# Kernel tuning notes

Measured on AMD Instinct MI355X. Metric: run time of the kernel, lower is better.

## Reference

```python
import jax, jax.numpy as jnp
import numpy as np

# Multi-scale feature pyramid (H, W) per level, standard Deformable-DETR for ~800x800 input
SHAPES = [(100, 100), (50, 50), (25, 25), (13, 13)]
D = 256      # d_model
NH = 8       # n_heads
NL = 4       # n_levels
NP = 4       # n_points
HD = D // NH # head_dim = 32
B = 2
S = sum(h * w for h, w in SHAPES)  # 13294
Lq = S  # encoder-style: one query per multi-scale token


def setup_inputs() -> dict:
    key = jax.random.key(0)
    ks = jax.random.split(key, 11)
    return {
        "query": jax.random.normal(ks[0], (B, Lq, D), jnp.float32),
        "reference_points": jax.random.uniform(ks[1], (B, Lq, NL, 2), jnp.float32),
        "value": jax.random.normal(ks[2], (B, S, D), jnp.float32),
        "W_val": jax.random.normal(ks[3], (D, D), jnp.float32) * 0.02,
        "b_val": jnp.zeros((D,), jnp.float32),
        "W_off": jax.random.normal(ks[4], (D, NH * NL * NP * 2), jnp.float32) * 0.01,
        "b_off": jax.random.normal(ks[5], (NH * NL * NP * 2,), jnp.float32) * 0.5,
        "W_attn": jax.random.normal(ks[6], (D, NH * NL * NP), jnp.float32) * 0.02,
        "b_attn": jnp.zeros((NH * NL * NP,), jnp.float32),
        "W_out": jax.random.normal(ks[7], (D, D), jnp.float32) * 0.02,
        "b_out": jnp.zeros((D,), jnp.float32),
    }


def _bilinear_sample(valf, x, y, H, W):
    """grid_sample(mode=bilinear, padding_mode=zeros, align_corners=False).
    valf: [N, H*W, C] flattened feature map; x, y: [N, P] pixel-space coords
    (already converted via x = loc_x*W - 0.5). Returns [N, P, C].
    """
    x0 = jnp.floor(x); y0 = jnp.floor(y)
    x1 = x0 + 1.0;     y1 = y0 + 1.0
    wx1 = x - x0; wx0 = 1.0 - wx1
    wy1 = y - y0; wy0 = 1.0 - wy1

    def corner(xi, yi, w):
        inb = (xi >= 0) & (xi <= W - 1) & (yi >= 0) & (yi <= H - 1)
        xi_c = jnp.clip(xi, 0, W - 1).astype(jnp.int32)
        yi_c = jnp.clip(yi, 0, H - 1).astype(jnp.int32)
        idx = yi_c * W + xi_c                                   # [N, P]
        v = jnp.take_along_axis(valf, idx[..., None], axis=1)   # [N, P, C]
        return v * (w * inb.astype(valf.dtype))[..., None]

    return (corner(x0, y0, wx0 * wy0) + corner(x1, y0, wx1 * wy0)
            + corner(x0, y1, wx0 * wy1) + corner(x1, y1, wx1 * wy1))


def reference(query, reference_points, value, W_val, b_val, W_off, b_off,
              W_attn, b_attn, W_out, b_out):
    Bq, L, _ = query.shape
    # value projection, split into heads: [B, S, NH, HD]
    val = (value @ W_val + b_val).reshape(Bq, S, NH, HD)
    # sampling offsets and attention weights from query
    offsets = (query @ W_off + b_off).reshape(Bq, L, NH, NL, NP, 2)
    w = (query @ W_attn + b_attn).reshape(Bq, L, NH, NL * NP)
    w = jax.nn.softmax(w, axis=-1).reshape(Bq, L, NH, NL, NP)
    # normalize offsets by (W, H) per level; 2D reference points path
    offset_norm = jnp.array([[wd, h] for h, wd in SHAPES], jnp.float32)  # [NL, 2]
    locs = (reference_points[:, :, None, :, None, :]
            + offsets / offset_norm[None, None, None, :, None, :])       # [B,L,NH,NL,NP,2]

    splits = [h * wd for h, wd in SHAPES]
    starts = np.concatenate([[0], np.cumsum(splits)])
    out_acc = jnp.zeros((Bq, L, NH, HD), query.dtype)
    for lvl, (H, W) in enumerate(SHAPES):
        vl = val[:, starts[lvl]:starts[lvl + 1]]                 # [B, HW, NH, HD]
        vl = vl.transpose(0, 2, 1, 3).reshape(Bq * NH, H * W, HD)
        loc = locs[:, :, :, lvl].transpose(0, 2, 1, 3, 4).reshape(Bq * NH, L * NP, 2)
        x = loc[..., 0] * W - 0.5   # align_corners=False pixel coords
        y = loc[..., 1] * H - 0.5
        s = _bilinear_sample(vl, x, y, H, W).reshape(Bq, NH, L, NP, HD)
        wl = w[:, :, :, lvl].transpose(0, 2, 1, 3)               # [B, NH, L, NP]
        out_acc = out_acc + jnp.einsum('bhqpd,bhqp->bqhd', s, wl)
    out = out_acc.reshape(Bq, L, NH * HD)
    return out @ W_out + b_out
```

## Files before the change

### kernel.cpp

```cpp
#include <hip/hip_runtime.h>
#include <hip/hip_bf16.h>
#include <math.h>

#define B_    2
#define NH_   8
#define NL_   4
#define NP_   4
#define HD_   32
#define S_    13294
#define L_    13294
#define M_    26588

__device__ __constant__ int c_H[NL_]     = {100, 50, 25, 13};
__device__ __constant__ int c_W[NL_]     = {100, 50, 25, 13};
__device__ __constant__ int c_start[NL_] = {0, 10000, 12500, 13125};

typedef __attribute__((ext_vector_type(8))) _Float16 f16x8;
typedef __attribute__((ext_vector_type(2))) _Float16 f16x2;
typedef __attribute__((ext_vector_type(4))) float    float4v;

__device__ __forceinline__ unsigned short f2h(float f) {
    _Float16 h = (_Float16)f;
    return __builtin_bit_cast(unsigned short, h);
}
__device__ __forceinline__ float h2f(unsigned short u) {
    _Float16 h = __builtin_bit_cast(_Float16, u);
    return (float)h;
}
__device__ __forceinline__ f16x2 pkrtz(float a, float b) {
    return __builtin_bit_cast(f16x2, __builtin_amdgcn_cvt_pkrtz(a, b));
}

__global__ __launch_bounds__(256) void prep_weights(
    const float* __restrict__ W_val, const float* __restrict__ W_off,
    const float* __restrict__ W_attn, const float* __restrict__ b_off,
    const float* __restrict__ b_attn, const float* __restrict__ W_out,
    unsigned short* __restrict__ wt_val, unsigned short* __restrict__ wt_oa,
    unsigned short* __restrict__ wt_out, float* __restrict__ bias_oa)
{
    int i = blockIdx.x * 256 + threadIdx.x;
    if (i < 65536) {
        int n = i >> 8, k = i & 255;
        wt_val[i] = f2h(W_val[k * 256 + n]);
    } else if (i < 65536 + 98304) {
        int j = i - 65536;
        int n = j >> 8, k = j & 255;
        float v = (n < 256) ? W_off[k * 256 + n] : W_attn[k * 128 + (n - 256)];
        wt_oa[j] = f2h(v);
    } else if (i < 65536 + 98304 + 65536) {
        int j = i - 163840;
        int n = j >> 8, k = j & 255;
        wt_out[j] = f2h(W_out[k * 256 + n]);
    } else if (i < 229376 + 384) {
        int j = i - 229376;
        bias_oa[j] = (j < 256) ? b_off[j] : b_attn[j - 256];
    }
}

template<int N, int OUT, bool AF32>
__device__ __forceinline__ void gemm_body(
    const void* __restrict__ Av,
    const unsigned short* __restrict__ WT,
    const float* __restrict__ bias,
    void* __restrict__ Cv,
    unsigned short (* __restrict__ As)[64][40])
{
    constexpr int NT = N / 64;

    const int tid  = threadIdx.x;
    const int lane = tid & 63;
    const int wave = tid >> 6;
    const int rowBase = blockIdx.x * 64;
    const int wcol = wave * (N / 4);

    const int ar   = tid >> 2;
    const int ako  = (tid & 3) * 8;
    const int grow = rowBase + ar;
    const int fr   = lane & 15;
    const int fk   = (lane >> 4) * 8;

    float4v acc[4][NT] = {};

    const unsigned short* bbase[NT];
#pragma unroll
    for (int t = 0; t < NT; ++t)
        bbase[t] = WT + (size_t)(wcol + t * 16 + fr) * 256 + fk;

    f16x8 curB[NT], nxtB[NT];
    float4 ra0, ra1;
    f16x8  rah;

    auto loadA = [&](int k0) {
        if constexpr (AF32) {
            const float* A = (const float*)Av;
            if (grow < M_) {
                ra0 = *reinterpret_cast<const float4*>(A + (size_t)grow * 256 + k0 + ako);
                ra1 = *reinterpret_cast<const float4*>(A + (size_t)grow * 256 + k0 + ako + 4);
            } else { ra0 = make_float4(0.f,0.f,0.f,0.f); ra1 = ra0; }
        } else {
            const unsigned short* A = (const unsigned short*)Av;
            if (grow < M_)
                rah = *reinterpret_cast<const f16x8*>(A + (size_t)grow * 256 + k0 + ako);
            else
                rah = f16x8{};
        }
    };
    auto storeA = [&](int buf) {
        f16x8 s;
        if constexpr (AF32) {
            f16x2 p0 = pkrtz(ra0.x, ra0.y);
            f16x2 p1 = pkrtz(ra0.z, ra0.w);
            f16x2 p2 = pkrtz(ra1.x, ra1.y);
            f16x2 p3 = pkrtz(ra1.z, ra1.w);
            s[0]=p0[0]; s[1]=p0[1]; s[2]=p1[0]; s[3]=p1[1];
            s[4]=p2[0]; s[5]=p2[1]; s[6]=p3[0]; s[7]=p3[1];
        } else {
            s = rah;
        }
        *reinterpret_cast<f16x8*>(&As[buf][ar][ako]) = s;
    };
    auto loadB = [&](f16x8* dst, int k0) {
#pragma unroll
        for (int t = 0; t < NT; ++t)
            dst[t] = *reinterpret_cast<const f16x8*>(bbase[t] + k0);
    };

    loadA(0);
    loadB(curB, 0);
    storeA(0);
    loadA(32);

#pragma unroll
    for (int it = 0; it < 8; ++it) {
        __syncthreads();
        f16x8 af[4];
#pragma unroll
        for (int t = 0; t < 4; ++t)
            af[t] = *reinterpret_cast<const f16x8*>(&As[it & 1][t * 16 + fr][fk]);
        if (it < 7) {
            storeA((it + 1) & 1);
            if (it < 6) loadA((it + 2) * 32);
            loadB(nxtB, (it + 1) * 32);
        }
#pragma unroll
        for (int mt = 0; mt < 4; ++mt)
#pragma unroll
            for (int nt = 0; nt < NT; ++nt)
                acc[mt][nt] = __builtin_amdgcn_mfma_f32_16x16x32_f16(
                    af[mt], curB[nt], acc[mt][nt], 0, 0, 0);
        if (it < 7) {
#pragma unroll
            for (int t = 0; t < NT; ++t) curB[t] = nxtB[t];
        }
    }

    const int dn  = lane & 15;
    const int dm0 = (lane >> 4) * 4;
#pragma unroll
    for (int mt = 0; mt < 4; ++mt) {
#pragma unroll
        for (int nt = 0; nt < NT; ++nt) {
            const int col = wcol + nt * 16 + dn;
            const float bv = bias[col];
#pragma unroll
            for (int r = 0; r < 4; ++r) {
                const int row = rowBase + mt * 16 + dm0 + r;
                if (row < M_) {
                    const float v = acc[mt][nt][r] + bv;
                    if constexpr (OUT == 0)
                        ((unsigned short*)Cv)[(size_t)row * 256 + col] = f2h(v);
                    else if constexpr (OUT == 1)
                        ((unsigned short*)Cv)[(size_t)row * 384 + col] = f2h(v);
                    else
                        ((float*)Cv)[(size_t)row * 256 + col] = v;
                }
            }
        }
    }
}

__global__ __launch_bounds__(256) void gemm_vq(
    const float* __restrict__ value, const float* __restrict__ query,
    const unsigned short* __restrict__ wt_val, const unsigned short* __restrict__ wt_oa,
    const float* __restrict__ b_val, const float* __restrict__ bias_oa,
    unsigned short* __restrict__ val_f16, unsigned short* __restrict__ oa_f16)
{
    __shared__ unsigned short As[2][64][40];
    if (blockIdx.y == 0)
        gemm_body<256, 0, true>(value, wt_val, b_val, val_f16, As);
    else
        gemm_body<384, 1, true>(query, wt_oa, bias_oa, oa_f16, As);
}

__global__ __launch_bounds__(256) void gemm_out3(
    const unsigned short* __restrict__ Af16,
    const unsigned short* __restrict__ WT,
    const float* __restrict__ bias, float* __restrict__ C)
{
    __shared__ unsigned short As[2][64][40];
    gemm_body<256, 2, false>(Af16, WT, bias, C, As);
}

__global__ __launch_bounds__(256) void deform_sample_v5(
    const unsigned short* __restrict__ val,
    const float* __restrict__ refp,
    const unsigned short* __restrict__ oa,
    unsigned short* __restrict__ acc)
{
    const int tid = threadIdx.x;
    const int q0  = blockIdx.x * 8;

    __shared__ unsigned short sLog[8][128];
    __shared__ float sMS[8][8][2];
    __shared__ int   sPack[8][4][16][8];

    {
        const int q  = tid >> 5;
        const int f  = tid & 31;
        const int bq = min(q0 + q, M_ - 1);
        *reinterpret_cast<int2*>(&sLog[q][f * 4]) =
            *reinterpret_cast<const int2*>(oa + (size_t)bq * 384 + 256 + f * 4);
    }
    __syncthreads();

    if (tid < 64) {
        const int q = tid >> 3, h = tid & 7;
        float m = -1e30f;
#pragma unroll
        for (int i = 0; i < 16; ++i) m = fmaxf(m, h2f(sLog[q][h * 16 + i]));
        float s = 0.f;
#pragma unroll
        for (int i = 0; i < 16; ++i) s += __expf(h2f(sLog[q][h * 16 + i]) - m);
        sMS[q][h][0] = m;
        sMS[q][h][1] = 1.f / s;
    }
    __syncthreads();

#pragma unroll
    for (int k = 0; k < 4; ++k) {
        const int e   = tid + k * 256;
        const int q   = e >> 7;
        const int t   = e & 127;
        const int h   = t >> 4;
        const int lp  = t & 15;
        const int lvl = lp >> 2;
        const int p   = lp & 3;
        const int bq  = min(q0 + q, M_ - 1);

        const float wgt = __expf(h2f(sLog[q][t]) - sMS[q][h][0]) * sMS[q][h][1];

        const int Wi = c_W[lvl], Hi = c_H[lvl], st = c_start[lvl];
        const float rx = refp[((size_t)bq * NL_ + lvl) * 2 + 0];
        const float ry = refp[((size_t)bq * NL_ + lvl) * 2 + 1];
        const float ox = h2f(oa[(size_t)bq * 384 + h * 32 + lvl * 8 + p * 2 + 0]);
        const float oy = h2f(oa[(size_t)bq * 384 + h * 32 + lvl * 8 + p * 2 + 1]);
        const float x = rx * (float)Wi + ox - 0.5f;
        const float y = ry * (float)Hi + oy - 0.5f;

        const float x0f = floorf(x), y0f = floorf(y);
        const int   x0 = (int)x0f,   y0 = (int)y0f;
        const float wx1 = x - x0f, wx0 = 1.f - wx1;
        const float wy1 = y - y0f, wy0 = 1.f - wy1;

        const int   cx[4] = {x0, x0 + 1, x0,     x0 + 1};
        const int   cy[4] = {y0, y0,     y0 + 1, y0 + 1};
        const float cw[4] = {wx0 * wy0, wx1 * wy0, wx0 * wy1, wx1 * wy1};
#pragma unroll
        for (int c = 0; c < 4; ++c) {
            const bool inb = (cx[c] >= 0) & (cx[c] < Wi) & (cy[c] >= 0) & (cy[c] < Hi);
            const int xi = min(max(cx[c], 0), Wi - 1);
            const int yi = min(max(cy[c], 0), Hi - 1);
            const int idx = st + yi * Wi + xi;
            const unsigned short wh = f2h(inb ? wgt * cw[c] : 0.f);
            sPack[q][c][lp][h] = idx | ((int)wh << 16);
        }
    }
    __syncthreads();

    const int q  = tid >> 5;
    const int h  = (tid >> 2) & 7;
    const int d4 = tid & 3;
    const int bq = q0 + q;
    const int b  = min(bq, M_ - 1) / L_;
    const unsigned short* vb = val + (size_t)b * S_ * 256 + h * 32 + d4 * 8;

    f16x2 A0{}, A1{}, A2{}, A3{};
#pragma unroll 8
    for (int i = 0; i < 64; ++i) {
        const int lp = i >> 2;
        const int c  = i & 3;
        const int pk = sPack[q][c][lp][h];
        const unsigned wb = (unsigned)pk >> 16;
        const f16x2 w2 = __builtin_bit_cast(f16x2, (wb << 16) | wb);
        const int4 u = *reinterpret_cast<const int4*>(
            vb + (size_t)((unsigned)pk & 0xffffu) * 256);
        A0 += w2 * __builtin_bit_cast(f16x2, u.x);
        A1 += w2 * __builtin_bit_cast(f16x2, u.y);
        A2 += w2 * __builtin_bit_cast(f16x2, u.z);
        A3 += w2 * __builtin_bit_cast(f16x2, u.w);
    }
    if (bq < M_) {
        int4 o;
        o.x = __builtin_bit_cast(int, A0);
        o.y = __builtin_bit_cast(int, A1);
        o.z = __builtin_bit_cast(int, A2);
        o.w = __builtin_bit_cast(int, A3);
        *reinterpret_cast<int4*>(acc + (size_t)bq * 256 + h * 32 + d4 * 8) = o;
    }
}

extern "C" void kernel_launch(void* const* d_in, const int* in_sizes, int n_in,
                              void* d_out, int out_size, void* d_ws, size_t ws_size,
                              hipStream_t stream) {
    const float* query  = (const float*)d_in[0];
    const float* refp   = (const float*)d_in[1];
    const float* value  = (const float*)d_in[2];
    const float* W_val  = (const float*)d_in[3];
    const float* b_val  = (const float*)d_in[4];
    const float* W_off  = (const float*)d_in[5];
    const float* b_off  = (const float*)d_in[6];
    const float* W_attn = (const float*)d_in[7];
    const float* b_attn = (const float*)d_in[8];
    const float* W_out  = (const float*)d_in[9];
    const float* b_out  = (const float*)d_in[10];
    float* out = (float*)d_out;

    char* ws = (char*)d_ws;
    const size_t mb = (size_t)M_ * 256;
    unsigned short* val_f16 = (unsigned short*)ws;  ws += mb * 2;
    unsigned short* acc_f16 = (unsigned short*)ws;  ws += mb * 2;
    unsigned short* oa_f16  = (unsigned short*)ws;  ws += (size_t)M_ * 384 * 2;
    unsigned short* wt_val  = (unsigned short*)ws;  ws += 65536 * 2;
    unsigned short* wt_oa   = (unsigned short*)ws;  ws += 98304 * 2;
    unsigned short* wt_out  = (unsigned short*)ws;  ws += 65536 * 2;
    float*          bias_oa = (float*)ws;           ws += 384 * 4;

    dim3 blk(256);

    prep_weights<<<dim3(898), blk, 0, stream>>>(
        W_val, W_off, W_attn, b_off, b_attn, W_out, wt_val, wt_oa, wt_out, bias_oa);

    gemm_vq<<<dim3((M_ + 63) / 64, 2), blk, 0, stream>>>(
        value, query, wt_val, wt_oa, b_val, bias_oa, val_f16, oa_f16);

    deform_sample_v5<<<dim3((M_ + 7) / 8), blk, 0, stream>>>(val_f16, refp, oa_f16, acc_f16);

    gemm_out3<<<dim3((M_ + 63) / 64), blk, 0, stream>>>(acc_f16, wt_out, b_out, out);
}
```

Before: 207.3 us.

## Fuse offset/attention projection, deformable sampling and output projection into one kernel

Replaces the separate query-projection GEMM, sampling kernel and output GEMM with one kernel that works on 16 queries per block. It projects the query into offsets and logits in shared memory, runs softmax and bilinear sampling in two halves of 8 queries, then applies the output projection straight from shared memory. This removes the global round trips for the offset/logit buffer and the sampled accumulator. The value projection becomes its own kernel with 32-row tiles. The cost is that each block now streams the full weight matrices for only 16 rows, which gives little B reuse, and the block uses more shared memory, which may lower occupancy.

```diff
diff --git a/kernel.cpp b/kernel.cpp
--- a/kernel.cpp
+++ b/kernel.cpp
@@ -16,6 +16,7 @@
 __device__ __constant__ int c_start[NL_] = {0, 10000, 12500, 13125};
 
 typedef __attribute__((ext_vector_type(8))) _Float16 f16x8;
+typedef __attribute__((ext_vector_type(4))) _Float16 f16x4;
 typedef __attribute__((ext_vector_type(2))) _Float16 f16x2;
 typedef __attribute__((ext_vector_type(4))) float    float4v;
 
@@ -57,255 +58,315 @@
     }
 }
 
-template<int N, int OUT, bool AF32>
-__device__ __forceinline__ void gemm_body(
-    const void* __restrict__ Av,
-    const unsigned short* __restrict__ WT,
-    const float* __restrict__ bias,
-    void* __restrict__ Cv,
-    unsigned short (* __restrict__ As)[64][40])
+__global__ __launch_bounds__(256, 4) void val_proj(
+    const float* __restrict__ value,
+    const unsigned short* __restrict__ wt_val,
+    const float* __restrict__ b_val,
+    unsigned short* __restrict__ val_f16)
 {
-    constexpr int NT = N / 64;
+    __shared__ unsigned short As[2][32][40];
 
     const int tid  = threadIdx.x;
     const int lane = tid & 63;
     const int wave = tid >> 6;
-    const int rowBase = blockIdx.x * 64;
-    const int wcol = wave * (N / 4);
-
-    const int ar   = tid >> 2;
-    const int ako  = (tid & 3) * 8;
-    const int grow = rowBase + ar;
-    const int fr   = lane & 15;
-    const int fk   = (lane >> 4) * 8;
-
-    float4v acc[4][NT] = {};
-
-    const unsigned short* bbase[NT];
-#pragma unroll
-    for (int t = 0; t < NT; ++t)
-        bbase[t] = WT + (size_t)(wcol + t * 16 + fr) * 256 + fk;
-
-    f16x8 curB[NT], nxtB[NT];
-    float4 ra0, ra1;
-    f16x8  rah;
-
-    auto loadA = [&](int k0) {
-        if constexpr (AF32) {
-            const float* A = (const float*)Av;
-            if (grow < M_) {
-                ra0 = *reinterpret_cast<const float4*>(A + (size_t)grow * 256 + k0 + ako);
-                ra1 = *reinterpret_cast<const float4*>(A + (size_t)grow * 256 + k0 + ako + 4);
-            } else { ra0 = make_float4(0.f,0.f,0.f,0.f); ra1 = ra0; }
-        } else {
-            const unsigned short* A = (const unsigned short*)Av;
-            if (grow < M_)
-                rah = *reinterpret_cast<const f16x8*>(A + (size_t)grow * 256 + k0 + ako);
-            else
-                rah = f16x8{};
-        }
+    const int rowBase = blockIdx.x * 32;
+    const int wcol = wave * 64;
+
+    const int r  = tid >> 3;
+    const int ko = (tid & 7) * 4;
+    int arow = rowBase + r; if (arow >= M_) arow = M_ - 1;
+    const float* aptr = value + (size_t)arow * 256 + ko;
+
+    const int fr = lane & 15;
+    const int fk = (lane >> 4) * 8;
+
+    const unsigned short* bb[4];
+#pragma unroll
+    for (int t = 0; t < 4; ++t)
+        bb[t] = wt_val + (size_t)(wcol + t * 16 + fr) * 256 + fk;
+
+    float4 ra[4];
+    f16x8 curB[4], nxtB[4];
+    float4v acc[2][4] = {};
+
+    auto stA = [&](int slot, int buf) {
+        f16x2 p0 = pkrtz(ra[slot].x, ra[slot].y);
+        f16x2 p1 = pkrtz(ra[slot].z, ra[slot].w);
+        f16x4 v; v[0] = p0[0]; v[1] = p0[1]; v[2] = p1[0]; v[3] = p1[1];
+        *reinterpret_cast<f16x4*>(&As[buf][r][ko]) = v;
     };
-    auto storeA = [&](int buf) {
-        f16x8 s;
-        if constexpr (AF32) {
-            f16x2 p0 = pkrtz(ra0.x, ra0.y);
-            f16x2 p1 = pkrtz(ra0.z, ra0.w);
-            f16x2 p2 = pkrtz(ra1.x, ra1.y);
-            f16x2 p3 = pkrtz(ra1.z, ra1.w);
-            s[0]=p0[0]; s[1]=p0[1]; s[2]=p1[0]; s[3]=p1[1];
-            s[4]=p2[0]; s[5]=p2[1]; s[6]=p3[0]; s[7]=p3[1];
-        } else {
-            s = rah;
-        }
-        *reinterpret_cast<f16x8*>(&As[buf][ar][ako]) = s;
-    };
-    auto loadB = [&](f16x8* dst, int k0) {
-#pragma unroll
-        for (int t = 0; t < NT; ++t)
-            dst[t] = *reinterpret_cast<const f16x8*>(bbase[t] + k0);
-    };
-
-    loadA(0);
-    loadB(curB, 0);
-    storeA(0);
-    loadA(32);
+
+#pragma unroll
+    for (int c = 0; c < 4; ++c)
+        ra[c] = *reinterpret_cast<const float4*>(aptr + c * 32);
+#pragma unroll
+    for (int t = 0; t < 4; ++t)
+        curB[t] = *reinterpret_cast<const f16x8*>(bb[t]);
+    stA(0, 0);
 
 #pragma unroll
     for (int it = 0; it < 8; ++it) {
         __syncthreads();
-        f16x8 af[4];
-#pragma unroll
-        for (int t = 0; t < 4; ++t)
-            af[t] = *reinterpret_cast<const f16x8*>(&As[it & 1][t * 16 + fr][fk]);
+        f16x8 af0 = *reinterpret_cast<const f16x8*>(&As[it & 1][fr][fk]);
+        f16x8 af1 = *reinterpret_cast<const f16x8*>(&As[it & 1][16 + fr][fk]);
         if (it < 7) {
-            storeA((it + 1) & 1);
-            if (it < 6) loadA((it + 2) * 32);
-            loadB(nxtB, (it + 1) * 32);
-        }
-#pragma unroll
-        for (int mt = 0; mt < 4; ++mt)
-#pragma unroll
-            for (int nt = 0; nt < NT; ++nt)
-                acc[mt][nt] = __builtin_amdgcn_mfma_f32_16x16x32_f16(
-                    af[mt], curB[nt], acc[mt][nt], 0, 0, 0);
+            stA((it + 1) & 3, (it + 1) & 1);
+            if (it < 4)
+                ra[(it + 4) & 3] = *reinterpret_cast<const float4*>(aptr + (it + 4) * 32);
+#pragma unroll
+            for (int t = 0; t < 4; ++t)
+                nxtB[t] = *reinterpret_cast<const f16x8*>(bb[t] + (it + 1) * 32);
+        }
+#pragma unroll
+        for (int nt = 0; nt < 4; ++nt) {
+            acc[0][nt] = __builtin_amdgcn_mfma_f32_16x16x32_f16(af0, curB[nt], acc[0][nt], 0, 0, 0);
+            acc[1][nt] = __builtin_amdgcn_mfma_f32_16x16x32_f16(af1, curB[nt], acc[1][nt], 0, 0, 0);
+        }
         if (it < 7) {
 #pragma unroll
-            for (int t = 0; t < NT; ++t) curB[t] = nxtB[t];
+            for (int t = 0; t < 4; ++t) curB[t] = nxtB[t];
         }
     }
 
     const int dn  = lane & 15;
     const int dm0 = (lane >> 4) * 4;
 #pragma unroll
-    for (int mt = 0; mt < 4; ++mt) {
-#pragma unroll
-        for (int nt = 0; nt < NT; ++nt) {
+    for (int mt = 0; mt < 2; ++mt)
+#pragma unroll
+        for (int nt = 0; nt < 4; ++nt) {
             const int col = wcol + nt * 16 + dn;
-            const float bv = bias[col];
-#pragma unroll
-            for (int r = 0; r < 4; ++r) {
-                const int row = rowBase + mt * 16 + dm0 + r;
-                if (row < M_) {
-                    const float v = acc[mt][nt][r] + bv;
-                    if constexpr (OUT == 0)
-                        ((unsigned short*)Cv)[(size_t)row * 256 + col] = f2h(v);
-                    else if constexpr (OUT == 1)
-                        ((unsigned short*)Cv)[(size_t)row * 384 + col] = f2h(v);
-                    else
-                        ((float*)Cv)[(size_t)row * 256 + col] = v;
-                }
-            }
-        }
-    }
-}
-
-__global__ __launch_bounds__(256) void gemm_vq(
-    const float* __restrict__ value, const float* __restrict__ query,
-    const unsigned short* __restrict__ wt_val, const unsigned short* __restrict__ wt_oa,
-    const float* __restrict__ b_val, const float* __restrict__ bias_oa,
-    unsigned short* __restrict__ val_f16, unsigned short* __restrict__ oa_f16)
+            const float bv = b_val[col];
+#pragma unroll
+            for (int rr = 0; rr < 4; ++rr) {
+                const int row = rowBase + mt * 16 + dm0 + rr;
+                if (row < M_)
+                    val_f16[(size_t)row * 256 + col] = f2h(acc[mt][nt][rr] + bv);
+            }
+        }
+}
+
+__global__ __launch_bounds__(256, 4) void mega(
+    const unsigned short* __restrict__ val,
+    const float* __restrict__ query,
+    const float* __restrict__ refp,
+    const unsigned short* __restrict__ wt_oa,
+    const unsigned short* __restrict__ wt_out,
+    const float* __restrict__ bias_oa,
+    const float* __restrict__ b_out,
+    float* __restrict__ out)
 {
-    __shared__ unsigned short As[2][64][40];
-    if (blockIdx.y == 0)
-        gemm_body<256, 0, true>(value, wt_val, b_val, val_f16, As);
-    else
-        gemm_body<384, 1, true>(query, wt_oa, bias_oa, oa_f16, As);
-}
-
-__global__ __launch_bounds__(256) void gemm_out3(
-    const unsigned short* __restrict__ Af16,
-    const unsigned short* __restrict__ WT,
-    const float* __restrict__ bias, float* __restrict__ C)
-{
-    __shared__ unsigned short As[2][64][40];
-    gemm_body<256, 2, false>(Af16, WT, bias, C, As);
-}
-
-__global__ __launch_bounds__(256) void deform_sample_v5(
-    const unsigned short* __restrict__ val,
-    const float* __restrict__ refp,
-    const unsigned short* __restrict__ oa,
-    unsigned short* __restrict__ acc)
-{
-    const int tid = threadIdx.x;
-    const int q0  = blockIdx.x * 8;
-
-    __shared__ unsigned short sLog[8][128];
-    __shared__ float sMS[8][8][2];
+    const int tid  = threadIdx.x;
+    const int lane = tid & 63;
+    const int wave = tid >> 6;
+    const int q0   = blockIdx.x * 16;
+
+    __shared__ unsigned short sQA[16][264];
+    __shared__ unsigned short sOA[16][384];
+    __shared__ float sMS[16][8][2];
     __shared__ int   sPack[8][4][16][8];
 
+    const int fr = lane & 15;
+    const int fk = (lane >> 4) * 8;
+    const int dn  = lane & 15;
+    const int dm0 = (lane >> 4) * 4;
+
     {
-        const int q  = tid >> 5;
-        const int f  = tid & 31;
-        const int bq = min(q0 + q, M_ - 1);
-        *reinterpret_cast<int2*>(&sLog[q][f * 4]) =
-            *reinterpret_cast<const int2*>(oa + (size_t)bq * 384 + 256 + f * 4);
+        const int r = tid >> 4;
+        const int c = (tid & 15) * 16;
+        const int bq = min(q0 + r, M_ - 1);
+        const float* qp = query + (size_t)bq * 256 + c;
+        float4 f0 = *reinterpret_cast<const float4*>(qp);
+        float4 f1 = *reinterpret_cast<const float4*>(qp + 4);
+        float4 f2 = *reinterpret_cast<const float4*>(qp + 8);
+        float4 f3 = *reinterpret_cast<const float4*>(qp + 12);
+        f16x8 h0, h1;
+        f16x2 p;
+        p = pkrtz(f0.x, f0.y); h0[0] = p[0]; h0[1] = p[1];
+        p = pkrtz(f0.z, f0.w); h0[2] = p[0]; h0[3] = p[1];
+        p = pkrtz(f1.x, f1.y); h0[4] = p[0]; h0[5] = p[1];
+        p = pkrtz(f1.z, f1.w); h0[6] = p[0]; h0[7] = p[1];
+        p = pkrtz(f2.x, f2.y); h1[0] = p[0]; h1[1] = p[1];
+        p = pkrtz(f2.z, f2.w); h1[2] = p[0]; h1[3] = p[1];
+        p = pkrtz(f3.x, f3.y); h1[4] = p[0]; h1[5] = p[1];
+        p = pkrtz(f3.z, f3.w); h1[6] = p[0]; h1[7] = p[1];
+        *reinterpret_cast<f16x8*>(&sQA[r][c]) = h0;
+        *reinterpret_cast<f16x8*>(&sQA[r][c + 8]) = h1;
     }
     __syncthreads();
 
-    if (tid < 64) {
+    {
+        const int wcol = wave * 96;
+        const unsigned short* bb[6];
+#pragma unroll
+        for (int t = 0; t < 6; ++t)
+            bb[t] = wt_oa + (size_t)(wcol + t * 16 + fr) * 256 + fk;
+
+        float4v aoa[6] = {};
+        f16x8 curB[6], nxtB[6];
+#pragma unroll
+        for (int t = 0; t < 6; ++t)
+            curB[t] = *reinterpret_cast<const f16x8*>(bb[t]);
+
+#pragma unroll
+        for (int ki = 0; ki < 8; ++ki) {
+            f16x8 af = *reinterpret_cast<const f16x8*>(&sQA[fr][fk + 32 * ki]);
+            if (ki < 7) {
+#pragma unroll
+                for (int t = 0; t < 6; ++t)
+                    nxtB[t] = *reinterpret_cast<const f16x8*>(bb[t] + (ki + 1) * 32);
+            }
+#pragma unroll
+            for (int t = 0; t < 6; ++t)
+                aoa[t] = __builtin_amdgcn_mfma_f32_16x16x32_f16(af, curB[t], aoa[t], 0, 0, 0);
+            if (ki < 7) {
+#pragma unroll
+                for (int t = 0; t < 6; ++t) curB[t] = nxtB[t];
+            }
+        }
+        __syncthreads();
+#pragma unroll
+        for (int t = 0; t < 6; ++t) {
+            const int col = wcol + t * 16 + dn;
+            const float bv = bias_oa[col];
+#pragma unroll
+            for (int rr = 0; rr < 4; ++rr)
+                sOA[dm0 + rr][col] = f2h(aoa[t][rr] + bv);
+        }
+    }
+    __syncthreads();
+
+    if (tid < 128) {
         const int q = tid >> 3, h = tid & 7;
         float m = -1e30f;
 #pragma unroll
-        for (int i = 0; i < 16; ++i) m = fmaxf(m, h2f(sLog[q][h * 16 + i]));
+        for (int i = 0; i < 16; ++i) m = fmaxf(m, h2f(sOA[q][256 + h * 16 + i]));
         float s = 0.f;
 #pragma unroll
-        for (int i = 0; i < 16; ++i) s += __expf(h2f(sLog[q][h * 16 + i]) - m);
+        for (int i = 0; i < 16; ++i) s += __expf(h2f(sOA[q][256 + h * 16 + i]) - m);
         sMS[q][h][0] = m;
         sMS[q][h][1] = 1.f / s;
     }
     __syncthreads();
 
-#pragma unroll
-    for (int k = 0; k < 4; ++k) {
-        const int e   = tid + k * 256;
-        const int q   = e >> 7;
-        const int t   = e & 127;
-        const int h   = t >> 4;
-        const int lp  = t & 15;
-        const int lvl = lp >> 2;
-        const int p   = lp & 3;
-        const int bq  = min(q0 + q, M_ - 1);
-
-        const float wgt = __expf(h2f(sLog[q][t]) - sMS[q][h][0]) * sMS[q][h][1];
-
-        const int Wi = c_W[lvl], Hi = c_H[lvl], st = c_start[lvl];
-        const float rx = refp[((size_t)bq * NL_ + lvl) * 2 + 0];
-        const float ry = refp[((size_t)bq * NL_ + lvl) * 2 + 1];
-        const float ox = h2f(oa[(size_t)bq * 384 + h * 32 + lvl * 8 + p * 2 + 0]);
-        const float oy = h2f(oa[(size_t)bq * 384 + h * 32 + lvl * 8 + p * 2 + 1]);
-        const float x = rx * (float)Wi + ox - 0.5f;
-        const float y = ry * (float)Hi + oy - 0.5f;
-
-        const float x0f = floorf(x), y0f = floorf(y);
-        const int   x0 = (int)x0f,   y0 = (int)y0f;
-        const float wx1 = x - x0f, wx0 = 1.f - wx1;
-        const float wy1 = y - y0f, wy0 = 1.f - wy1;
-
-        const int   cx[4] = {x0, x0 + 1, x0,     x0 + 1};
-        const int   cy[4] = {y0, y0,     y0 + 1, y0 + 1};
-        const float cw[4] = {wx0 * wy0, wx1 * wy0, wx0 * wy1, wx1 * wy1};
-#pragma unroll
-        for (int c = 0; c < 4; ++c) {
-            const bool inb = (cx[c] >= 0) & (cx[c] < Wi) & (cy[c] >= 0) & (cy[c] < Hi);
-            const int xi = min(max(cx[c], 0), Wi - 1);
-            const int yi = min(max(cy[c], 0), Hi - 1);
-            const int idx = st + yi * Wi + xi;
-            const unsigned short wh = f2h(inb ? wgt * cw[c] : 0.f);
-            sPack[q][c][lp][h] = idx | ((int)wh << 16);
-        }
-    }
-    __syncthreads();
-
-    const int q  = tid >> 5;
-    const int h  = (tid >> 2) & 7;
-    const int d4 = tid & 3;
-    const int bq = q0 + q;
-    const int b  = min(bq, M_ - 1) / L_;
-    const unsigned short* vb = val + (size_t)b * S_ * 256 + h * 32 + d4 * 8;
-
-    f16x2 A0{}, A1{}, A2{}, A3{};
+#pragma unroll 1
+    for (int half = 0; half < 2; ++half) {
+#pragma unroll
+        for (int k = 0; k < 4; ++k) {
+            const int e   = tid + k * 256;
+            const int q8  = e >> 7;
+            const int t   = e & 127;
+            const int q   = half * 8 + q8;
+            const int h   = t >> 4;
+            const int lp  = t & 15;
+            const int lvl = lp >> 2;
+            const int p   = lp & 3;
+            const int bq  = min(q0 + q, M_ - 1);
+
+            const float wgt = __expf(h2f(sOA[q][256 + t]) - sMS[q][h][0]) * sMS[q][h][1];
+
+            const int Wi = c_W[lvl], Hi = c_H[lvl], st = c_start[lvl];
+            const float rx = refp[((size_t)bq * NL_ + lvl) * 2 + 0];
+            const float ry = refp[((size_t)bq * NL_ + lvl) * 2 + 1];
+            const float ox = h2f(sOA[q][h * 32 + lvl * 8 + p * 2 + 0]);
+            const float oy = h2f(sOA[q][h * 32 + lvl * 8 + p * 2 + 1]);
+            const float x = rx * (float)Wi + ox - 0.5f;
+            const float y = ry * (float)Hi + oy - 0.5f;
+
+            const float x0f = floorf(x), y0f = floorf(y);
+            const int   x0 = (int)x0f,   y0 = (int)y0f;
+            const float wx1 = x - x0f, wx0 = 1.f - wx1;
+            const float wy1 = y - y0f, wy0 = 1.f - wy1;
+
+            const int   cx[4] = {x0, x0 + 1, x0,     x0 + 1};
+            const int   cy[4] = {y0, y0,     y0 + 1, y0 + 1};
+            const float cw[4] = {wx0 * wy0, wx1 * wy0, wx0 * wy1, wx1 * wy1};
+#pragma unroll
+            for (int c = 0; c < 4; ++c) {
+                const bool inb = (cx[c] >= 0) & (cx[c] < Wi) & (cy[c] >= 0) & (cy[c] < Hi);
+                const int xi = min(max(cx[c], 0), Wi - 1);
+                const int yi = min(max(cy[c], 0), Hi - 1);
+                const int idx = st + yi * Wi + xi;
+                const unsigned short wh = f2h(inb ? wgt * cw[c] : 0.f);
+                sPack[q8][c][lp][h] = idx | ((int)wh << 16);
+            }
+        }
+        __syncthreads();
+
+        {
+            const int q8 = tid >> 5;
+            const int q  = half * 8 + q8;
+            const int h  = (tid >> 2) & 7;
+            const int d4 = tid & 3;
+            const int bq = q0 + q;
+            const int b  = min(bq, M_ - 1) / L_;
+            const unsigned short* vb = val + (size_t)b * S_ * 256 + h * 32 + d4 * 8;
+
+            f16x2 A0{}, A1{}, A2{}, A3{};
 #pragma unroll 8
-    for (int i = 0; i < 64; ++i) {
-        const int lp = i >> 2;
-        const int c  = i & 3;
-        const int pk = sPack[q][c][lp][h];
-        const unsigned wb = (unsigned)pk >> 16;
-        const f16x2 w2 = __builtin_bit_cast(f16x2, (wb << 16) | wb);
-        const int4 u = *reinterpret_cast<const int4*>(
-            vb + (size_t)((unsigned)pk & 0xffffu) * 256);
-        A0 += w2 * __builtin_bit_cast(f16x2, u.x);
-        A1 += w2 * __builtin_bit_cast(f16x2, u.y);
-        A2 += w2 * __builtin_bit_cast(f16x2, u.z);
-        A3 += w2 * __builtin_bit_cast(f16x2, u.w);
-    }
-    if (bq < M_) {
-        int4 o;
-        o.x = __builtin_bit_cast(int, A0);
-        o.y = __builtin_bit_cast(int, A1);
-        o.z = __builtin_bit_cast(int, A2);
-        o.w = __builtin_bit_cast(int, A3);
-        *reinterpret_cast<int4*>(acc + (size_t)bq * 256 + h * 32 + d4 * 8) = o;
+            for (int i = 0; i < 64; ++i) {
+                const int lp = i >> 2;
+                const int c  = i & 3;
+                const int pk = sPack[q8][c][lp][h];
+                const unsigned wb = (unsigned)pk >> 16;
+                const f16x2 w2 = __builtin_bit_cast(f16x2, (wb << 16) | wb);
+                const int4 u = *reinterpret_cast<const int4*>(
+                    vb + (size_t)((unsigned)pk & 0xffffu) * 256);
+                A0 += w2 * __builtin_bit_cast(f16x2, u.x);
+                A1 += w2 * __builtin_bit_cast(f16x2, u.y);
+                A2 += w2 * __builtin_bit_cast(f16x2, u.z);
+                A3 += w2 * __builtin_bit_cast(f16x2, u.w);
+            }
+            int4 o;
+            o.x = __builtin_bit_cast(int, A0);
+            o.y = __builtin_bit_cast(int, A1);
+            o.z = __builtin_bit_cast(int, A2);
+            o.w = __builtin_bit_cast(int, A3);
+            *reinterpret_cast<int4*>(&sQA[q][h * 32 + d4 * 8]) = o;
+        }
+        __syncthreads();
+    }
+
+    {
+        const int wcol = wave * 64;
+        const unsigned short* bb[4];
+#pragma unroll
+        for (int t = 0; t < 4; ++t)
+            bb[t] = wt_out + (size_t)(wcol + t * 16 + fr) * 256 + fk;
+
+        float4v ao[4] = {};
+        f16x8 curB[4], nxtB[4];
+#pragma unroll
+        for (int t = 0; t < 4; ++t)
+            curB[t] = *reinterpret_cast<const f16x8*>(bb[t]);
+
+#pragma unroll
+        for (int ki = 0; ki < 8; ++ki) {
+            f16x8 af = *reinterpret_cast<const f16x8*>(&sQA[fr][fk + 32 * ki]);
+            if (ki < 7) {
+#pragma unroll
+                for (int t = 0; t < 4; ++t)
+                    nxtB[t] = *reinterpret_cast<const f16x8*>(bb[t] + (ki + 1) * 32);
+            }
+#pragma unroll
+            for (int t = 0; t < 4; ++t)
+                ao[t] = __builtin_amdgcn_mfma_f32_16x16x32_f16(af, curB[t], ao[t], 0, 0, 0);
+            if (ki < 7) {
+#pragma unroll
+                for (int t = 0; t < 4; ++t) curB[t] = nxtB[t];
+            }
+        }
+
+#pragma unroll
+        for (int t = 0; t < 4; ++t) {
+            const int col = wcol + t * 16 + dn;
+            const float bv = b_out[col];
+#pragma unroll
+            for (int rr = 0; rr < 4; ++rr) {
+                const int bq = q0 + dm0 + rr;
+                if (bq < M_)
+                    out[(size_t)bq * 256 + col] = ao[t][rr] + bv;
+            }
+        }
     }
 }
 
@@ -328,8 +389,6 @@
     char* ws = (char*)d_ws;
     const size_t mb = (size_t)M_ * 256;
     unsigned short* val_f16 = (unsigned short*)ws;  ws += mb * 2;
-    unsigned short* acc_f16 = (unsigned short*)ws;  ws += mb * 2;
-    unsigned short* oa_f16  = (unsigned short*)ws;  ws += (size_t)M_ * 384 * 2;
     unsigned short* wt_val  = (unsigned short*)ws;  ws += 65536 * 2;
     unsigned short* wt_oa   = (unsigned short*)ws;  ws += 98304 * 2;
     unsigned short* wt_out  = (unsigned short*)ws;  ws += 65536 * 2;
@@ -340,10 +399,8 @@
     prep_weights<<<dim3(898), blk, 0, stream>>>(
         W_val, W_off, W_attn, b_off, b_attn, W_out, wt_val, wt_oa, wt_out, bias_oa);
 
-    gemm_vq<<<dim3((M_ + 63) / 64, 2), blk, 0, stream>>>(
-        value, query, wt_val, wt_oa, b_val, bias_oa, val_f16, oa_f16);
-
-    deform_sample_v5<<<dim3((M_ + 7) / 8), blk, 0, stream>>>(val_f16, refp, oa_f16, acc_f16);
-
-    gemm_out3<<<dim3((M_ + 63) / 64), blk, 0, stream>>>(acc_f16, wt_out, b_out, out);
-}
+    val_proj<<<dim3((M_ + 31) / 32), blk, 0, stream>>>(value, wt_val, b_val, val_f16);
+
+    mega<<<dim3((M_ + 15) / 16), blk, 0, stream>>>(
+        val_f16, query, refp, wt_oa, wt_out, bias_oa, b_out, out);
+}
```

After: 233.2 us. 12.5% more time.

## Halve GEMM row tile to 32 and prefetch all A chunks up front

Applied to the files above, without the earlier changes.

The shared GEMM body now tiles 32 rows per block instead of 64, doubling the grid for the value/query projections and the output projection. A-tile loads are reorganised so each thread holds four float4 slots, with the first four K-chunks issued at the start and the rest loaded in a rolling ring. This gives more blocks and deeper load prefetch to hide latency, at the cost of re-reading the B weights from L2 twice as often and doing less MFMA work per B fetch. Out-of-range rows are clamped to the last valid row rather than zero-filled, and their stores are still masked.

```diff
diff --git a/kernel.cpp b/kernel.cpp
--- a/kernel.cpp
+++ b/kernel.cpp
@@ -16,6 +16,7 @@
 __device__ __constant__ int c_start[NL_] = {0, 10000, 12500, 13125};
 
 typedef __attribute__((ext_vector_type(8))) _Float16 f16x8;
+typedef __attribute__((ext_vector_type(4))) _Float16 f16x4;
 typedef __attribute__((ext_vector_type(2))) _Float16 f16x2;
 typedef __attribute__((ext_vector_type(4))) float    float4v;
 
@@ -58,96 +59,83 @@
 }
 
 template<int N, int OUT, bool AF32>
-__device__ __forceinline__ void gemm_body(
+__device__ __forceinline__ void gemm32_body(
     const void* __restrict__ Av,
     const unsigned short* __restrict__ WT,
     const float* __restrict__ bias,
     void* __restrict__ Cv,
-    unsigned short (* __restrict__ As)[64][40])
+    unsigned short (* __restrict__ As)[32][40])
 {
     constexpr int NT = N / 64;
 
     const int tid  = threadIdx.x;
     const int lane = tid & 63;
     const int wave = tid >> 6;
-    const int rowBase = blockIdx.x * 64;
+    const int rowBase = blockIdx.x * 32;
     const int wcol = wave * (N / 4);
 
-    const int ar   = tid >> 2;
-    const int ako  = (tid & 3) * 8;
-    const int grow = rowBase + ar;
-    const int fr   = lane & 15;
-    const int fk   = (lane >> 4) * 8;
-
-    float4v acc[4][NT] = {};
-
-    const unsigned short* bbase[NT];
+    const int r  = tid >> 3;
+    const int ko = (tid & 7) * 4;
+    int arow = rowBase + r; if (arow >= M_) arow = M_ - 1;
+
+    const int fr = lane & 15;
+    const int fk = (lane >> 4) * 8;
+
+    const unsigned short* bb[NT];
 #pragma unroll
     for (int t = 0; t < NT; ++t)
-        bbase[t] = WT + (size_t)(wcol + t * 16 + fr) * 256 + fk;
-
+        bb[t] = WT + (size_t)(wcol + t * 16 + fr) * 256 + fk;
+
+    float4 raf[4];
+    f16x4  rah[4];
     f16x8 curB[NT], nxtB[NT];
-    float4 ra0, ra1;
-    f16x8  rah;
-
-    auto loadA = [&](int k0) {
+    float4v acc[2][NT] = {};
+
+    auto ldA = [&](int slot, int bk) {
         if constexpr (AF32) {
-            const float* A = (const float*)Av;
-            if (grow < M_) {
-                ra0 = *reinterpret_cast<const float4*>(A + (size_t)grow * 256 + k0 + ako);
-                ra1 = *reinterpret_cast<const float4*>(A + (size_t)grow * 256 + k0 + ako + 4);
-            } else { ra0 = make_float4(0.f,0.f,0.f,0.f); ra1 = ra0; }
+            raf[slot] = *reinterpret_cast<const float4*>(
+                (const float*)Av + (size_t)arow * 256 + bk * 32 + ko);
         } else {
-            const unsigned short* A = (const unsigned short*)Av;
-            if (grow < M_)
-                rah = *reinterpret_cast<const f16x8*>(A + (size_t)grow * 256 + k0 + ako);
-            else
-                rah = f16x8{};
+            rah[slot] = *reinterpret_cast<const f16x4*>(
+                (const unsigned short*)Av + (size_t)arow * 256 + bk * 32 + ko);
         }
     };
-    auto storeA = [&](int buf) {
-        f16x8 s;
+    auto stA = [&](int slot, int buf) {
+        f16x4 v;
         if constexpr (AF32) {
-            f16x2 p0 = pkrtz(ra0.x, ra0.y);
-            f16x2 p1 = pkrtz(ra0.z, ra0.w);
-            f16x2 p2 = pkrtz(ra1.x, ra1.y);
-            f16x2 p3 = pkrtz(ra1.z, ra1.w);
-            s[0]=p0[0]; s[1]=p0[1]; s[2]=p1[0]; s[3]=p1[1];
-            s[4]=p2[0]; s[5]=p2[1]; s[6]=p3[0]; s[7]=p3[1];
+            f16x2 p0 = pkrtz(raf[slot].x, raf[slot].y);
+            f16x2 p1 = pkrtz(raf[slot].z, raf[slot].w);
+            v[0] = p0[0]; v[1] = p0[1]; v[2] = p1[0]; v[3] = p1[1];
         } else {
-            s = rah;
-        }
-        *reinterpret_cast<f16x8*>(&As[buf][ar][ako]) = s;
+            v = rah[slot];
+        }
+        *reinterpret_cast<f16x4*>(&As[buf][r][ko]) = v;
     };
-    auto loadB = [&](f16x8* dst, int k0) {
-#pragma unroll
-        for (int t = 0; t < NT; ++t)
-            dst[t] = *reinterpret_cast<const f16x8*>(bbase[t] + k0);
-    };
-
-    loadA(0);
-    loadB(curB, 0);
-    storeA(0);
-    loadA(32);
+
+#pragma unroll
+    for (int c = 0; c < 4; ++c) ldA(c, c);
+#pragma unroll
+    for (int t = 0; t < NT; ++t)
+        curB[t] = *reinterpret_cast<const f16x8*>(bb[t]);
+    stA(0, 0);
 
 #pragma unroll
     for (int it = 0; it < 8; ++it) {
         __syncthreads();
-        f16x8 af[4];
-#pragma unroll
-        for (int t = 0; t < 4; ++t)
-            af[t] = *reinterpret_cast<const f16x8*>(&As[it & 1][t * 16 + fr][fk]);
+        f16x8 af0 = *reinterpret_cast<const f16x8*>(&As[it & 1][fr][fk]);
+        f16x8 af1 = *reinterpret_cast<const f16x8*>(&As[it & 1][16 + fr][fk]);
         if (it < 7) {
-            storeA((it + 1) & 1);
-            if (it < 6) loadA((it + 2) * 32);
-            loadB(nxtB, (it + 1) * 32);
-        }
-#pragma unroll
-        for (int mt = 0; mt < 4; ++mt)
-#pragma unroll
-            for (int nt = 0; nt < NT; ++nt)
-                acc[mt][nt] = __builtin_amdgcn_mfma_f32_16x16x32_f16(
-                    af[mt], curB[nt], acc[mt][nt], 0, 0, 0);
+            stA((it + 1) & 3, (it + 1) & 1);
+            if (it < 4) ldA(it & 3, it + 4);
+#pragma unroll
+            for (int t = 0; t < NT; ++t)
+                nxtB[t] = *reinterpret_cast<const f16x8*>(bb[t] + (it + 1) * 32);
+        }
+#pragma unroll
+        for (int nt = 0; nt < NT; ++nt) {
+            acc[0][nt] = __builtin_amdgcn_mfma_f32_16x16x32_f16(af0, curB[nt], acc[0][nt], 0, 0, 0);
+            acc[1][nt] = __builtin_amdgcn_mfma_f32_16x16x32_f16(af1, curB[nt], acc[1][nt], 0, 0, 0);
+        }
         if (it < 7) {
 #pragma unroll
             for (int t = 0; t < NT; ++t) curB[t] = nxtB[t];
@@ -157,16 +145,16 @@
     const int dn  = lane & 15;
     const int dm0 = (lane >> 4) * 4;
 #pragma unroll
-    for (int mt = 0; mt < 4; ++mt) {
+    for (int mt = 0; mt < 2; ++mt)
 #pragma unroll
         for (int nt = 0; nt < NT; ++nt) {
             const int col = wcol + nt * 16 + dn;
             const float bv = bias[col];
 #pragma unroll
-            for (int r = 0; r < 4; ++r) {
-                const int row = rowBase + mt * 16 + dm0 + r;
+            for (int rr = 0; rr < 4; ++rr) {
+                const int row = rowBase + mt * 16 + dm0 + rr;
                 if (row < M_) {
-                    const float v = acc[mt][nt][r] + bv;
+                    const float v = acc[mt][nt][rr] + bv;
                     if constexpr (OUT == 0)
                         ((unsigned short*)Cv)[(size_t)row * 256 + col] = f2h(v);
                     else if constexpr (OUT == 1)
@@ -176,7 +164,6 @@
                 }
             }
         }
-    }
 }
 
 __global__ __launch_bounds__(256) void gemm_vq(
@@ -185,20 +172,20 @@
     const float* __restrict__ b_val, const float* __restrict__ bias_oa,
     unsigned short* __restrict__ val_f16, unsigned short* __restrict__ oa_f16)
 {
-    __shared__ unsigned short As[2][64][40];
+    __shared__ unsigned short As[2][32][40];
     if (blockIdx.y == 0)
-        gemm_body<256, 0, true>(value, wt_val, b_val, val_f16, As);
+        gemm32_body<256, 0, true>(value, wt_val, b_val, val_f16, As);
     else
-        gemm_body<384, 1, true>(query, wt_oa, bias_oa, oa_f16, As);
-}
-
-__global__ __launch_bounds__(256) void gemm_out3(
+        gemm32_body<384, 1, true>(query, wt_oa, bias_oa, oa_f16, As);
+}
+
+__global__ __launch_bounds__(256) void gemm_out4(
     const unsigned short* __restrict__ Af16,
     const unsigned short* __restrict__ WT,
     const float* __restrict__ bias, float* __restrict__ C)
 {
-    __shared__ unsigned short As[2][64][40];
-    gemm_body<256, 2, false>(Af16, WT, bias, C, As);
+    __shared__ unsigned short As[2][32][40];
+    gemm32_body<256, 2, false>(Af16, WT, bias, C, As);
 }
 
 __global__ __launch_bounds__(256) void deform_sample_v5(
@@ -340,10 +327,10 @@
     prep_weights<<<dim3(898), blk, 0, stream>>>(
         W_val, W_off, W_attn, b_off, b_attn, W_out, wt_val, wt_oa, wt_out, bias_oa);
 
-    gemm_vq<<<dim3((M_ + 63) / 64, 2), blk, 0, stream>>>(
+    gemm_vq<<<dim3((M_ + 31) / 32, 2), blk, 0, stream>>>(
         value, query, wt_val, wt_oa, b_val, bias_oa, val_f16, oa_f16);
 
     deform_sample_v5<<<dim3((M_ + 7) / 8), blk, 0, stream>>>(val_f16, refp, oa_f16, acc_f16);
 
-    gemm_out3<<<dim3((M_ + 63) / 64), blk, 0, stream>>>(acc_f16, wt_out, b_out, out);
-}
+    gemm_out4<<<dim3((M_ + 31) / 32), blk, 0, stream>>>(acc_f16, wt_out, b_out, out);
+}
```

Result: slower. 226.3 us (+9.2%).
